# Kernel tuning notes

Measured on AMD Instinct MI355X. Metric: run time of the kernel, lower is better.

## Reference

```python
import jax, jax.numpy as jnp
import numpy as np

B, T, E, H = 1, 4096, 1024, 16
HD = E // H  # 64
SCALE = 8.0 / HD  # scaling='d' per Tensor Programs V


def setup_inputs() -> dict:
    key = jax.random.key(0)
    ks = jax.random.split(key, 7)
    s = 1.0 / np.sqrt(E)
    return {
        "q": jax.random.normal(ks[0], (B, T, E), jnp.float32),
        "k": jax.random.normal(ks[1], (B, T, E), jnp.float32),
        "v": jax.random.normal(ks[2], (B, T, E), jnp.float32),
        "Wq": jax.random.normal(ks[3], (E, E), jnp.float32) * s,
        "Wk": jax.random.normal(ks[4], (E, E), jnp.float32) * s,
        "Wv": jax.random.normal(ks[5], (E, E), jnp.float32) * s,
        "Wo": jax.random.normal(ks[6], (E, E), jnp.float32) * s,
    }


def reference(q, k, v, Wq, Wk, Wv, Wo):
    # bias-free linear projections (nn.Linear: y = x @ W.T)
    qp = q @ Wq.T
    kp = k @ Wk.T
    vp = v @ Wv.T
    # b t (h d) -> b h t d
    qh = qp.reshape(B, T, H, HD).transpose(0, 2, 1, 3)
    kh = kp.reshape(B, T, H, HD).transpose(0, 2, 1, 3)
    vh = vp.reshape(B, T, H, HD).transpose(0, 2, 1, 3)
    scores = jnp.einsum('bhqd,bhkd->bhqk', qh, kh) * SCALE
    # causal mask: positions k > q masked with -inf
    causal = jnp.tril(jnp.ones((T, T), dtype=bool))
    scores = jnp.where(causal[None, None], scores, -jnp.inf)
    probs = jax.nn.softmax(scores, axis=-1)
    out = jnp.einsum('bhqk,bhkd->bhqd', probs, vh)
    # b h t d -> b t (h d)
    out = out.transpose(0, 2, 1, 3).reshape(B, T, E)
    return out @ Wo.T
```

## Files before the change

### kernel.cpp

```cpp
#include <hip/hip_runtime.h>
#include <hip/hip_bf16.h>

#define T_DIM 4096
#define E_DIM 1024
#define H_DIM 16
#define HD_DIM 64
#define LOG2E_F 1.4426950408889634f
#define QSCALE_F (0.125f * LOG2E_F)

typedef __bf16 bf16_t;
typedef __bf16 bf16x8 __attribute__((ext_vector_type(8)));
typedef float  f32x4  __attribute__((ext_vector_type(4)));

__device__ inline void stage8(bf16_t* dst, const float* src) {
  const f32x4* s4 = (const f32x4*)src;
  f32x4 a = s4[0], b = s4[1];
  bf16x8 o;
  o[0] = (bf16_t)a[0]; o[1] = (bf16_t)a[1]; o[2] = (bf16_t)a[2]; o[3] = (bf16_t)a[3];
  o[4] = (bf16_t)b[0]; o[5] = (bf16_t)b[1]; o[6] = (bf16_t)b[2]; o[7] = (bf16_t)b[3];
  *(bf16x8*)dst = o;
}
__device__ inline void stage8(bf16_t* dst, const bf16_t* src) {
  *(bf16x8*)dst = *(const bf16x8*)src;
}

__device__ inline void gld_lds16(const bf16_t* g, bf16_t* l) {
  __builtin_amdgcn_global_load_lds(
      (const __attribute__((address_space(1))) unsigned int*)g,
      (__attribute__((address_space(3))) unsigned int*)l, 16, 0, 0);
}

__device__ inline float fexp2(float x) {
  float r;
  asm("v_exp_f32 %0, %1" : "=v"(r) : "v"(x));
  return r;
}

__device__ inline void block_sync() {
  asm volatile("" ::: "memory");
  __builtin_amdgcn_s_barrier();
  asm volatile("" ::: "memory");
}

__global__ __launch_bounds__(256) void cvt_all(
    const float* __restrict__ q, const float* __restrict__ k, const float* __restrict__ v,
    const float* __restrict__ Wq, const float* __restrict__ Wk,
    const float* __restrict__ Wv, const float* __restrict__ Wo,
    bf16_t* qb, bf16_t* kb, bf16_t* vb,
    bf16_t* Wqb, bf16_t* Wkb, bf16_t* Wvb, bf16_t* Wob) {
  for (int u = blockIdx.x * 256 + threadIdx.x; u < 2097152; u += gridDim.x * 256) {
    const float* s; bf16_t* d; int i;
    if (u < 1572864) {
      int seg = u >> 19, off = u & 524287;
      s = seg == 0 ? q : (seg == 1 ? k : v);
      d = seg == 0 ? qb : (seg == 1 ? kb : vb);
      i = off;
    } else {
      int w = u - 1572864;
      int seg = w >> 17, off = w & 131071;
      s = seg == 0 ? Wq : seg == 1 ? Wk : seg == 2 ? Wv : Wo;
      d = seg == 0 ? Wqb : seg == 1 ? Wkb : seg == 2 ? Wvb : Wob;
      i = off;
    }
    stage8(d + (size_t)i * 8, s + (size_t)i * 8);
  }
}

template <int MF, int NF, typename TC>
__device__ __forceinline__ void gemm_body(const bf16_t* __restrict__ A,
                                          const bf16_t* __restrict__ B,
                                          TC* __restrict__ C,
                                          int ldC, int bm, int bn, float cs) {
  constexpr int BM = 32 * MF, BN = 32 * NF;
  __shared__ alignas(16) bf16_t As[BM][64];
  __shared__ alignas(16) bf16_t Bs[BN][64];
  const int tid  = threadIdx.x;
  const int lane = tid & 63, w = tid >> 6;
  const int g = lane >> 4, l15 = lane & 15;
  const int wr = w >> 1, wc = w & 1;

  f32x4 acc[MF][NF] = {};

  for (int kt = 0; kt < 1024; kt += 64) {
    if (kt) __syncthreads();
#pragma unroll
    for (int p = 0; p < MF; ++p) {
      int s = p * 256 + tid;
      int row = s >> 3, c = s & 7;
      int cg = c ^ (row & 7);
      gld_lds16(&A[(size_t)(bm + row) * 1024 + kt + cg * 8], &As[0][0] + s * 8);
    }
#pragma unroll
    for (int p = 0; p < NF; ++p) {
      int s = p * 256 + tid;
      int row = s >> 3, c = s & 7;
      int cg = c ^ (row & 7);
      gld_lds16(&B[(size_t)(bn + row) * 1024 + kt + cg * 8], &Bs[0][0] + s * 8);
    }
    asm volatile("s_waitcnt vmcnt(0)" ::: "memory");
    __syncthreads();

#pragma unroll
    for (int hh = 0; hh < 2; ++hh) {
      bf16x8 af[MF], bfr[NF];
#pragma unroll
      for (int m = 0; m < MF; ++m) {
        int row = wr * (16 * MF) + m * 16 + l15;
        af[m] = *(const bf16x8*)(&As[0][0] + row * 64 + (((hh * 4 + g) ^ (row & 7)) * 8));
      }
#pragma unroll
      for (int n = 0; n < NF; ++n) {
        int row = wc * (16 * NF) + n * 16 + l15;
        bfr[n] = *(const bf16x8*)(&Bs[0][0] + row * 64 + (((hh * 4 + g) ^ (row & 7)) * 8));
      }
#pragma unroll
      for (int m = 0; m < MF; ++m)
#pragma unroll
        for (int n = 0; n < NF; ++n)
          acc[m][n] = __builtin_amdgcn_mfma_f32_16x16x32_bf16(af[m], bfr[n], acc[m][n], 0, 0, 0);
    }
  }

#pragma unroll
  for (int m = 0; m < MF; ++m)
#pragma unroll
    for (int n = 0; n < NF; ++n)
#pragma unroll
      for (int r = 0; r < 4; ++r) {
        int row = bm + wr * (16 * MF) + m * 16 + g * 4 + r;
        int col = bn + wc * (16 * NF) + n * 16 + l15;
        C[(size_t)row * ldC + col] = (TC)(acc[m][n][r] * cs);
      }
}

__global__ __launch_bounds__(256) void proj_qkv(
    const bf16_t* __restrict__ qb, const bf16_t* __restrict__ kb,
    const bf16_t* __restrict__ vb,
    const bf16_t* __restrict__ Wqb, const bf16_t* __restrict__ Wkb,
    const bf16_t* __restrict__ Wvb,
    bf16_t* Qp, bf16_t* Kp, bf16_t* Vt) {
  const int bid = blockIdx.x;
  const int which = bid >> 8, t = bid & 255;
  const bf16_t *A, *B; bf16_t* C; int ldC, bm, bn; float cs;
  if (which == 0) {
    A = qb;  B = Wqb; C = Qp; ldC = 1024;
    bm = (t >> 3) * 128; bn = (t & 7) * 128; cs = QSCALE_F;
  } else if (which == 1) {
    A = kb;  B = Wkb; C = Kp; ldC = 1024;
    bm = (t >> 3) * 128; bn = (t & 7) * 128; cs = 1.0f;
  } else {
    A = Wvb; B = vb;  C = Vt; ldC = 4096;
    bm = (t >> 5) * 128; bn = (t & 31) * 128; cs = 1.0f;
  }
  gemm_body<4, 4, bf16_t>(A, B, C, ldC, bm, bn, cs);
}

__global__ __launch_bounds__(256) void gemm_fin(const bf16_t* __restrict__ A,
                                                const bf16_t* __restrict__ B,
                                                float* __restrict__ C) {
  gemm_body<2, 4, float>(A, B, C, 1024, blockIdx.y * 64, blockIdx.x * 128, 1.0f);
}

template <typename TA, typename TB, typename TC>
__global__ __launch_bounds__(256) void gemm_bt(const TA* __restrict__ A,
                                               const TB* __restrict__ B,
                                               TC* __restrict__ C,
                                               int M, int N, int K, float cscale) {
  __shared__ alignas(16) bf16_t As[128][40];
  __shared__ alignas(16) bf16_t Bs[128][40];
  const int tid  = threadIdx.x;
  const int lane = tid & 63, w = tid >> 6;
  const int g = lane >> 4, l15 = lane & 15;
  const int wr = w >> 1, wc = w & 1;
  const int bm = blockIdx.y * 128, bn = blockIdx.x * 128;

  f32x4 acc[4][4] = {};

  for (int kt = 0; kt < K; kt += 32) {
    __syncthreads();
#pragma unroll
    for (int i = 0; i < 2; ++i) {
      int vv  = tid + i * 256;
      int row = vv >> 2, c8 = (vv & 3) * 8;
      stage8(&As[row][c8], &A[(size_t)(bm + row) * K + kt + c8]);
      stage8(&Bs[row][c8], &B[(size_t)(bn + row) * K + kt + c8]);
    }
    __syncthreads();

    bf16x8 af[4], bfr[4];
#pragma unroll
    for (int m = 0; m < 4; ++m)
      af[m] = *(const bf16x8*)&As[wr * 64 + m * 16 + l15][g * 8];
#pragma unroll
    for (int n = 0; n < 4; ++n)
      bfr[n] = *(const bf16x8*)&Bs[wc * 64 + n * 16 + l15][g * 8];
#pragma unroll
    for (int m = 0; m < 4; ++m)
#pragma unroll
      for (int n = 0; n < 4; ++n)
        acc[m][n] = __builtin_amdgcn_mfma_f32_16x16x32_bf16(af[m], bfr[n], acc[m][n], 0, 0, 0);
  }

#pragma unroll
  for (int m = 0; m < 4; ++m)
#pragma unroll
    for (int n = 0; n < 4; ++n)
#pragma unroll
      for (int r = 0; r < 4; ++r) {
        int row = bm + wr * 64 + m * 16 + g * 4 + r;
        int col = bn + wc * 64 + n * 16 + l15;
        C[(size_t)row * N + col] = (TC)(acc[m][n][r] * cscale);
      }
}

template <int CTRL>
__device__ inline float dpp_rot(float x) {
  return __builtin_bit_cast(float,
      __builtin_amdgcn_update_dpp(0, __builtin_bit_cast(int, x), CTRL, 0xF, 0xF, true));
}
__device__ inline float red_max16(float x) {
  x = fmaxf(x, dpp_rot<0x121>(x));
  x = fmaxf(x, dpp_rot<0x122>(x));
  x = fmaxf(x, dpp_rot<0x124>(x));
  x = fmaxf(x, dpp_rot<0x128>(x));
  return x;
}
__device__ inline float red_sum16(float x) {
  x += dpp_rot<0x121>(x);
  x += dpp_rot<0x122>(x);
  x += dpp_rot<0x124>(x);
  x += dpp_rot<0x128>(x);
  return x;
}

__global__ __launch_bounds__(256) void attn_fwd(const bf16_t* __restrict__ Qp,
                                                const bf16_t* __restrict__ Kp,
                                                const bf16_t* __restrict__ Vt,
                                                bf16_t* __restrict__ Oattn) {
  const int bid = blockIdx.x;
  const int h  = bid & 15;
  const int qi = 63 - (bid >> 4);
  const int tid = threadIdx.x, lane = tid & 63, w = tid >> 6;
  const int g = lane >> 4, l15 = lane & 15;
  const int qrow = qi * 64 + w * 16;

  __shared__ alignas(16) bf16_t Ks[2][64][64];
  __shared__ alignas(16) bf16_t Vs[3][64][64];
  __shared__ alignas(16) bf16_t Plds[4][16][72];

  bf16x8 qf[2];
  {
    const bf16_t* qp = &Qp[(size_t)(qrow + l15) * E_DIM + h * 64 + g * 8];
    qf[0] = *(const bf16x8*)qp;
    qf[1] = *(const bf16x8*)(qp + 32);
  }

  const int row0 = tid >> 3, c0 = tid & 7;
  const int cgo = (c0 ^ (row0 & 7)) * 8;
  const bf16_t* srcK0 = Kp + (size_t)row0 * E_DIM + h * 64 + cgo;
  const bf16_t* srcK1 = srcK0 + (size_t)32 * E_DIM;
  const bf16_t* srcV0 = Vt + (size_t)(h * 64 + row0) * T_DIM + cgo;
  const bf16_t* srcV1 = srcV0 + (size_t)32 * T_DIM;
  bf16_t* KsAll = &Ks[0][0][0];
  bf16_t* VsAll = &Vs[0][0][0];
  const size_t KADV = (size_t)64 * E_DIM;
  const int nt = qi + 1;

  auto issue = [&](int t) {
    bf16_t* kd = KsAll + (t & 1) * 4096;
    bf16_t* vd = VsAll + (t % 3) * 4096;
    gld_lds16(srcK0 + (size_t)t * KADV, kd + tid * 8);
    gld_lds16(srcK1 + (size_t)t * KADV, kd + (256 + tid) * 8);
    gld_lds16(srcV0 + (size_t)t * 64,   vd + tid * 8);
    gld_lds16(srcV1 + (size_t)t * 64,   vd + (256 + tid) * 8);
  };

  f32x4 acc[4] = {};
  float m_r[4], l_p[4];
#pragma unroll
  for (int r = 0; r < 4; ++r) { m_r[r] = -1e30f; l_p[r] = 0.f; }

  auto pv = [&](int t) {
    const char* Vb = (const char*)(VsAll + (t % 3) * 4096);
    bf16x8 pf0 = *(const bf16x8*)&Plds[w][l15][g * 8];
    bf16x8 pf1 = *(const bf16x8*)&Plds[w][l15][32 + g * 8];
#pragma unroll
    for (int c = 0; c < 4; ++c) {
      const int vr = c * 16 + l15;
      const char* rp = Vb + vr * 128;
      const int sw = (vr & 7) << 4;
      bf16x8 v0 = *(const bf16x8*)(rp + ((g * 16) ^ sw));
      bf16x8 v1 = *(const bf16x8*)(rp + ((64 + g * 16) ^ sw));
      acc[c] = __builtin_amdgcn_mfma_f32_16x16x32_bf16(pf0, v0, acc[c], 0, 0, 0);
      acc[c] = __builtin_amdgcn_mfma_f32_16x16x32_bf16(pf1, v1, acc[c], 0, 0, 0);
    }
  };

  issue(0);

  for (int j = 0; j < nt; ++j) {
    asm volatile("s_waitcnt vmcnt(0)" ::: "memory");
    block_sync();
    if (j + 1 < nt) issue(j + 1);

    __builtin_amdgcn_s_setprio(1);
    if (j > 0) pv(j - 1);

    const char* Kb = (const char*)(KsAll + (j & 1) * 4096);
    f32x4 s[4] = {};
#pragma unroll
    for (int j16 = 0; j16 < 4; ++j16) {
      const int r0 = j16 * 16 + l15;
      const char* rp = Kb + r0 * 128;
      const int sw = (r0 & 7) << 4;
      bf16x8 k0 = *(const bf16x8*)(rp + ((g * 16) ^ sw));
      bf16x8 k1 = *(const bf16x8*)(rp + ((64 + g * 16) ^ sw));
      s[j16] = __builtin_amdgcn_mfma_f32_16x16x32_bf16(qf[0], k0, s[j16], 0, 0, 0);
      s[j16] = __builtin_amdgcn_mfma_f32_16x16x32_bf16(qf[1], k1, s[j16], 0, 0, 0);
    }
    __builtin_amdgcn_s_setprio(0);

    if (j == nt - 1) {
      const int kb = j * 64;
#pragma unroll
      for (int j16 = 0; j16 < 4; ++j16)
#pragma unroll
        for (int r = 0; r < 4; ++r)
          if (kb + j16 * 16 + l15 > qrow + g * 4 + r) s[j16][r] = -1e30f;
    }

    float pmax[4];
#pragma unroll
    for (int r = 0; r < 4; ++r)
      pmax[r] = fmaxf(fmaxf(s[0][r], s[1][r]), fmaxf(s[2][r], s[3][r]));

    int stable = 1;
#pragma unroll
    for (int r = 0; r < 4; ++r) stable &= (pmax[r] <= m_r[r] + 11.0f);
    if (!__all(stable)) {
#pragma unroll
      for (int r = 0; r < 4; ++r) {
        float rm = red_max16(pmax[r]);
        float mn = fmaxf(m_r[r], rm);
        float sc = fexp2(m_r[r] - mn);
        m_r[r] = mn;
        l_p[r] *= sc;
#pragma unroll
        for (int c = 0; c < 4; ++c) acc[c][r] *= sc;
      }
    }

#pragma unroll
    for (int j16 = 0; j16 < 4; ++j16)
#pragma unroll
      for (int r = 0; r < 4; ++r)
        s[j16][r] = fexp2(s[j16][r] - m_r[r]);

#pragma unroll
    for (int r = 0; r < 4; ++r)
      l_p[r] += s[0][r] + s[1][r] + s[2][r] + s[3][r];

#pragma unroll
    for (int j16 = 0; j16 < 4; ++j16)
#pragma unroll
      for (int r = 0; r < 4; ++r)
        Plds[w][g * 4 + r][j16 * 16 + l15] = (bf16_t)s[j16][r];
  }

  pv(nt - 1);

  float l_row[4];
#pragma unroll
  for (int r = 0; r < 4; ++r) l_row[r] = red_sum16(l_p[r]);

#pragma unroll
  for (int c = 0; c < 4; ++c)
#pragma unroll
    for (int r = 0; r < 4; ++r) {
      float o = acc[c][r] / l_row[r];
      Oattn[(size_t)(qrow + g * 4 + r) * E_DIM + h * 64 + c * 16 + l15] = (bf16_t)o;
    }
}

extern "C" void kernel_launch(void* const* d_in, const int* in_sizes, int n_in,
                              void* d_out, int out_size, void* d_ws, size_t ws_size,
                              hipStream_t stream) {
  const float* q  = (const float*)d_in[0];
  const float* k  = (const float*)d_in[1];
  const float* v  = (const float*)d_in[2];
  const float* Wq = (const float*)d_in[3];
  const float* Wk = (const float*)d_in[4];
  const float* Wv = (const float*)d_in[5];
  const float* Wo = (const float*)d_in[6];
  float* out = (float*)d_out;

  const size_t TE = (size_t)T_DIM * E_DIM;
  const size_t EE = (size_t)E_DIM * E_DIM;
  dim3 blk(256);

  if (ws_size >= (size_t)56 * 1024 * 1024) {
    bf16_t* qb  = (bf16_t*)d_ws;
    bf16_t* kb  = qb + TE;
    bf16_t* vb  = kb + TE;
    bf16_t* Wqb = vb + TE;
    bf16_t* Wkb = Wqb + EE;
    bf16_t* Wvb = Wkb + EE;
    bf16_t* Wob = Wvb + EE;
    bf16_t* Qp  = Wob + EE;
    bf16_t* Kp  = Qp + TE;
    bf16_t* Vt  = Kp + TE;
    bf16_t* Oa  = qb;

    cvt_all<<<2048, blk, 0, stream>>>(q, k, v, Wq, Wk, Wv, Wo,
                                      qb, kb, vb, Wqb, Wkb, Wvb, Wob);
    proj_qkv<<<dim3(768), blk, 0, stream>>>(qb, kb, vb, Wqb, Wkb, Wvb, Qp, Kp, Vt);
    attn_fwd<<<dim3(1024), blk, 0, stream>>>(Qp, Kp, Vt, Oa);
    gemm_fin<<<dim3(8, 64), blk, 0, stream>>>(Oa, Wob, out);
  } else {
    bf16_t* Qp = (bf16_t*)d_ws;
    bf16_t* Kp = Qp + TE;
    bf16_t* Vt = Kp + TE;
    bf16_t* Oa = Vt + TE;
    gemm_bt<float, float, bf16_t><<<dim3(8, 32), blk, 0, stream>>>(q, Wq, Qp, T_DIM, E_DIM, E_DIM, QSCALE_F);
    gemm_bt<float, float, bf16_t><<<dim3(8, 32), blk, 0, stream>>>(k, Wk, Kp, T_DIM, E_DIM, E_DIM, 1.0f);
    gemm_bt<float, float, bf16_t><<<dim3(32, 8), blk, 0, stream>>>(Wv, v, Vt, E_DIM, T_DIM, E_DIM, 1.0f);
    attn_fwd<<<dim3(1024), blk, 0, stream>>>(Qp, Kp, Vt, Oa);
    gemm_bt<bf16_t, float, float><<<dim3(8, 32), blk, 0, stream>>>(Oa, Wo, out, T_DIM, E_DIM, E_DIM, 1.0f);
  }
}
```

Baseline: 142.4 us.

## Swap MFMA operand order so each lane owns one query row

The QK^T and PV MFMAs now take K/V as the A operand and Q/P as the B operand, so the accumulator is transposed and each lane holds a single query row. The per-row softmax max and sum become scalar per lane, reduced across the four lane groups with two xor shuffles instead of DPP reductions over four rows. The P tile writes to LDS and the output stores become vectorized 4-wide bf16 stores. Meant to cut the cross-lane reduction work, the rescale bookkeeping and the scalar LDS and global stores in the softmax inner loop. The causal mask indices are updated to match.

New measurement: 141.0 us. Within noise of the previous version (-1.0%).

```diff
diff --git a/kernel.cpp b/kernel.cpp
--- a/kernel.cpp
+++ b/kernel.cpp
@@ -10,6 +10,7 @@
 
 typedef __bf16 bf16_t;
 typedef __bf16 bf16x8 __attribute__((ext_vector_type(8)));
+typedef __bf16 bf16x4 __attribute__((ext_vector_type(4)));
 typedef float  f32x4  __attribute__((ext_vector_type(4)));
 
 __device__ inline void stage8(bf16_t* dst, const float* src) {
@@ -213,26 +214,6 @@
       }
 }
 
-template <int CTRL>
-__device__ inline float dpp_rot(float x) {
-  return __builtin_bit_cast(float,
-      __builtin_amdgcn_update_dpp(0, __builtin_bit_cast(int, x), CTRL, 0xF, 0xF, true));
-}
-__device__ inline float red_max16(float x) {
-  x = fmaxf(x, dpp_rot<0x121>(x));
-  x = fmaxf(x, dpp_rot<0x122>(x));
-  x = fmaxf(x, dpp_rot<0x124>(x));
-  x = fmaxf(x, dpp_rot<0x128>(x));
-  return x;
-}
-__device__ inline float red_sum16(float x) {
-  x += dpp_rot<0x121>(x);
-  x += dpp_rot<0x122>(x);
-  x += dpp_rot<0x124>(x);
-  x += dpp_rot<0x128>(x);
-  return x;
-}
-
 __global__ __launch_bounds__(256) void attn_fwd(const bf16_t* __restrict__ Qp,
                                                 const bf16_t* __restrict__ Kp,
                                                 const bf16_t* __restrict__ Vt,
@@ -276,9 +257,7 @@
   };
 
   f32x4 acc[4] = {};
-  float m_r[4], l_p[4];
-#pragma unroll
-  for (int r = 0; r < 4; ++r) { m_r[r] = -1e30f; l_p[r] = 0.f; }
+  float m_s = -1e30f, l_s = 0.f;
 
   auto pv = [&](int t) {
     const char* Vb = (const char*)(VsAll + (t % 3) * 4096);
@@ -291,8 +270,8 @@
       const int sw = (vr & 7) << 4;
       bf16x8 v0 = *(const bf16x8*)(rp + ((g * 16) ^ sw));
       bf16x8 v1 = *(const bf16x8*)(rp + ((64 + g * 16) ^ sw));
-      acc[c] = __builtin_amdgcn_mfma_f32_16x16x32_bf16(pf0, v0, acc[c], 0, 0, 0);
-      acc[c] = __builtin_amdgcn_mfma_f32_16x16x32_bf16(pf1, v1, acc[c], 0, 0, 0);
+      acc[c] = __builtin_amdgcn_mfma_f32_16x16x32_bf16(v0, pf0, acc[c], 0, 0, 0);
+      acc[c] = __builtin_amdgcn_mfma_f32_16x16x32_bf16(v1, pf1, acc[c], 0, 0, 0);
     }
   };
 
@@ -315,8 +294,8 @@
       const int sw = (r0 & 7) << 4;
       bf16x8 k0 = *(const bf16x8*)(rp + ((g * 16) ^ sw));
       bf16x8 k1 = *(const bf16x8*)(rp + ((64 + g * 16) ^ sw));
-      s[j16] = __builtin_amdgcn_mfma_f32_16x16x32_bf16(qf[0], k0, s[j16], 0, 0, 0);
-      s[j16] = __builtin_amdgcn_mfma_f32_16x16x32_bf16(qf[1], k1, s[j16], 0, 0, 0);
+      s[j16] = __builtin_amdgcn_mfma_f32_16x16x32_bf16(k0, qf[0], s[j16], 0, 0, 0);
+      s[j16] = __builtin_amdgcn_mfma_f32_16x16x32_bf16(k1, qf[1], s[j16], 0, 0, 0);
     }
     __builtin_amdgcn_s_setprio(0);
 
@@ -326,60 +305,59 @@
       for (int j16 = 0; j16 < 4; ++j16)
 #pragma unroll
         for (int r = 0; r < 4; ++r)
-          if (kb + j16 * 16 + l15 > qrow + g * 4 + r) s[j16][r] = -1e30f;
-    }
-
-    float pmax[4];
-#pragma unroll
-    for (int r = 0; r < 4; ++r)
-      pmax[r] = fmaxf(fmaxf(s[0][r], s[1][r]), fmaxf(s[2][r], s[3][r]));
-
-    int stable = 1;
-#pragma unroll
-    for (int r = 0; r < 4; ++r) stable &= (pmax[r] <= m_r[r] + 11.0f);
-    if (!__all(stable)) {
+          if (kb + j16 * 16 + g * 4 + r > qrow + l15) s[j16][r] = -1e30f;
+    }
+
+    float pmax = s[0][0];
+#pragma unroll
+    for (int j16 = 0; j16 < 4; ++j16)
+#pragma unroll
+      for (int r = 0; r < 4; ++r) pmax = fmaxf(pmax, s[j16][r]);
+    pmax = fmaxf(pmax, __shfl_xor(pmax, 16));
+    pmax = fmaxf(pmax, __shfl_xor(pmax, 32));
+
+    if (!__all(pmax <= m_s + 11.0f)) {
+      float mn = fmaxf(m_s, pmax);
+      float sc = fexp2(m_s - mn);
+      m_s = mn;
+      l_s *= sc;
+#pragma unroll
+      for (int c = 0; c < 4; ++c)
+#pragma unroll
+        for (int r = 0; r < 4; ++r) acc[c][r] *= sc;
+    }
+
+    float ps = 0.f;
+#pragma unroll
+    for (int j16 = 0; j16 < 4; ++j16)
 #pragma unroll
       for (int r = 0; r < 4; ++r) {
-        float rm = red_max16(pmax[r]);
-        float mn = fmaxf(m_r[r], rm);
-        float sc = fexp2(m_r[r] - mn);
-        m_r[r] = mn;
-        l_p[r] *= sc;
-#pragma unroll
-        for (int c = 0; c < 4; ++c) acc[c][r] *= sc;
+        s[j16][r] = fexp2(s[j16][r] - m_s);
+        ps += s[j16][r];
       }
-    }
-
-#pragma unroll
-    for (int j16 = 0; j16 < 4; ++j16)
-#pragma unroll
-      for (int r = 0; r < 4; ++r)
-        s[j16][r] = fexp2(s[j16][r] - m_r[r]);
-
-#pragma unroll
-    for (int r = 0; r < 4; ++r)
-      l_p[r] += s[0][r] + s[1][r] + s[2][r] + s[3][r];
-
-#pragma unroll
-    for (int j16 = 0; j16 < 4; ++j16)
-#pragma unroll
-      for (int r = 0; r < 4; ++r)
-        Plds[w][g * 4 + r][j16 * 16 + l15] = (bf16_t)s[j16][r];
+    ps += __shfl_xor(ps, 16);
+    ps += __shfl_xor(ps, 32);
+    l_s += ps;
+
+#pragma unroll
+    for (int j16 = 0; j16 < 4; ++j16) {
+      bf16x4 pk;
+      pk[0] = (bf16_t)s[j16][0]; pk[1] = (bf16_t)s[j16][1];
+      pk[2] = (bf16_t)s[j16][2]; pk[3] = (bf16_t)s[j16][3];
+      *(bf16x4*)&Plds[w][l15][j16 * 16 + g * 4] = pk;
+    }
   }
 
   pv(nt - 1);
 
-  float l_row[4];
-#pragma unroll
-  for (int r = 0; r < 4; ++r) l_row[r] = red_sum16(l_p[r]);
-
-#pragma unroll
-  for (int c = 0; c < 4; ++c)
-#pragma unroll
-    for (int r = 0; r < 4; ++r) {
-      float o = acc[c][r] / l_row[r];
-      Oattn[(size_t)(qrow + g * 4 + r) * E_DIM + h * 64 + c * 16 + l15] = (bf16_t)o;
-    }
+  const float inv = 1.0f / l_s;
+#pragma unroll
+  for (int c = 0; c < 4; ++c) {
+    bf16x4 o;
+#pragma unroll
+    for (int r = 0; r < 4; ++r) o[r] = (bf16_t)(acc[c][r] * inv);
+    *(bf16x4*)&Oattn[(size_t)(qrow + l15) * E_DIM + h * 64 + c * 16 + g * 4] = o;
+  }
 }
 
 extern "C" void kernel_launch(void* const* d_in, const int* in_sizes, int n_in,
```
